# Kernel optimization log

Hardware: AMD Instinct MI355X
Metric: run time of the kernel (lower is better)

## Reference

```python
import jax, jax.numpy as jnp
import numpy as np

B, H, S, D = 4, 32, 2048, 128  # batch, num_query_heads, seq_len, head_dim


def setup_inputs() -> dict:
    key = jax.random.key(0)
    k1, k2, k3, k4, k5 = jax.random.split(key, 5)
    return {
        "q": jax.random.normal(k1, (B, H, S, D), dtype=jnp.float32),
        "k": jax.random.normal(k2, (B, H, S, D), dtype=jnp.float32),
        "v": jax.random.normal(k3, (B, H, S, D), dtype=jnp.float32),
        "attention_output": jax.random.normal(k4, (B, H, S, D), dtype=jnp.float32),
        "betas": jnp.zeros((1, H, 1, D), dtype=jnp.float32),      # nn.Parameter(torch.zeros)
        "init_mem": jax.random.normal(k5, (1, H, D, D), dtype=jnp.float32),  # learnable init memory
        "init_z": jnp.ones((1, H, D, 1), dtype=jnp.float32),      # learnable init normalizer
    }


def reference(q, k, v, attention_output, betas, init_mem, init_z):
    # Infini-Attention style delta-rule memory, single segment (fresh init states).
    sigma_q = jax.nn.elu(q) + 1.0                      # [B,H,S,D]
    # memory read: [B,H,S,D] @ [1,H,D,D] -> [B,H,S,D], normalized by sigma_q @ z -> [B,H,S,1]
    memory_output = (sigma_q @ init_mem) / (sigma_q @ init_z)

    sigma_k = jax.nn.elu(k) + 1.0                      # [B,H,S,D]
    # delta rule: subtract what the memory already predicts for each key
    retrieved = (sigma_k @ init_mem) / (sigma_k @ init_z)
    value_delta = v - retrieved                        # [B,H,S,D]
    new_states = init_mem + jnp.swapaxes(sigma_k, -2, -1) @ value_delta  # [B,H,D,D]
    new_z = init_z + jnp.swapaxes(jnp.sum(sigma_k, axis=-2, keepdims=True), -2, -1)  # [B,H,D,1]

    gate = jax.nn.sigmoid(betas)                       # [1,H,1,D]
    out = gate * memory_output + (1.0 - gate) * attention_output
    # original returns only `out`; new_states/new_z are the side-effect state update,
    # returned here so the full delta-rule write path is exercised.
    return out, new_states, new_z
```

## Files before the change

kernel.cpp:

```cpp
#include <hip/hip_runtime.h>
#include <math.h>

#define NB 4
#define NH 32
#define NSQ 2048
#define ND 128
#define SPLIT 2
#define SCHUNK (NSQ / SPLIT)
#define RB 64
#define NITER (SCHUNK / RB)
#define NTHR 512

static constexpr size_t OUT_ELEMS = (size_t)NB * NH * NSQ * ND;
static constexpr size_t NS_OFF    = OUT_ELEMS;
static constexpr size_t NZ_OFF    = NS_OFF + (size_t)NB * NH * ND * ND;

static constexpr int LDS_BYTES = (2 * RB * 132 + 2 * ND * 64 + 3 * ND + 2 * RB) * 4;

typedef __attribute__((ext_vector_type(8))) short short8v;
typedef __attribute__((ext_vector_type(4))) float f32x4;

#define MFMA16(a, b, c) __builtin_amdgcn_mfma_f32_16x16x32_bf16(a, b, c, 0, 0, 0)

__device__ __forceinline__ float4 elu1(float4 x) {
    float4 r;
    r.x = x.x > 0.f ? x.x + 1.f : __expf(x.x);
    r.y = x.y > 0.f ? x.y + 1.f : __expf(x.y);
    r.z = x.z > 0.f ? x.z + 1.f : __expf(x.z);
    r.w = x.w > 0.f ? x.w + 1.f : __expf(x.w);
    return r;
}

__device__ __forceinline__ unsigned int pack1(float x) {
    unsigned int bx = __float_as_uint(x);
    float lo = x - __uint_as_float(bx & 0xFFFF0000u);
    return __builtin_amdgcn_perm(bx, __float_as_uint(lo), 0x07060302u);
}
__device__ __forceinline__ float uph(unsigned int w) { return __uint_as_float(w & 0xFFFF0000u); }
__device__ __forceinline__ float upl(unsigned int w) { return __uint_as_float(w << 16); }

__device__ __forceinline__ void unpack2(uint4 a, uint4 b, short8v& hi, short8v& lo) {
    union { unsigned int u[4]; short8v s; } H, L;
    H.u[0] = __builtin_amdgcn_perm(a.y, a.x, 0x07060302u);
    H.u[1] = __builtin_amdgcn_perm(a.w, a.z, 0x07060302u);
    H.u[2] = __builtin_amdgcn_perm(b.y, b.x, 0x07060302u);
    H.u[3] = __builtin_amdgcn_perm(b.w, b.z, 0x07060302u);
    L.u[0] = __builtin_amdgcn_perm(a.y, a.x, 0x05040100u);
    L.u[1] = __builtin_amdgcn_perm(a.w, a.z, 0x05040100u);
    L.u[2] = __builtin_amdgcn_perm(b.y, b.x, 0x05040100u);
    L.u[3] = __builtin_amdgcn_perm(b.w, b.z, 0x05040100u);
    hi = H.s; lo = L.s;
}

__device__ __forceinline__ void pack8(const float* x, short8v& hi, short8v& lo) {
    union { unsigned int u[4]; short8v s; } H, L;
    #pragma unroll
    for (int d = 0; d < 4; ++d) {
        unsigned int b0 = __float_as_uint(x[2 * d]);
        unsigned int b1 = __float_as_uint(x[2 * d + 1]);
        float l0 = x[2 * d]     - __uint_as_float(b0 & 0xFFFF0000u);
        float l1 = x[2 * d + 1] - __uint_as_float(b1 & 0xFFFF0000u);
        H.u[d] = __builtin_amdgcn_perm(b1, b0, 0x07060302u);
        L.u[d] = __builtin_amdgcn_perm(__float_as_uint(l1), __float_as_uint(l0), 0x07060302u);
    }
    hi = H.s; lo = L.s;
}

extern "C" __global__ void cm_init(const float* __restrict__ mem0,
                                   const float* __restrict__ z0,
                                   float* __restrict__ out) {
    const int NSF4 = NB * NH * ND * ND / 4;
    const int NZF4 = NB * NH * ND / 4;
    int idx = blockIdx.x * 256 + threadIdx.x;
    if (idx < NSF4) {
        const int per_bh = ND * ND / 4;
        int h = (idx / per_bh) % NH;
        int off = idx % per_bh;
        ((float4*)(out + NS_OFF))[idx] = ((const float4*)mem0)[h * per_bh + off];
    } else if (idx < NSF4 + NZF4) {
        int j = idx - NSF4;
        const int per_bh = ND / 4;
        int h = (j / per_bh) % NH;
        int off = j % per_bh;
        ((float4*)(out + NZ_OFF))[j] = ((const float4*)z0)[h * per_bh + off];
    }
}

extern "C" __global__ void __launch_bounds__(NTHR, 2)
cm_main(const float* __restrict__ q, const float* __restrict__ kin,
        const float* __restrict__ v, const float* __restrict__ attn,
        const float* __restrict__ betas, const float* __restrict__ mem0,
        const float* __restrict__ z0, float* __restrict__ out) {
    extern __shared__ unsigned int lds[];
    uint4* lsqT  = (uint4*)lds;
    uint4* lskT  = lsqT + RB * 33;
    uint4* skT   = lskT + RB * 33;
    uint4* vdT   = skT + ND * 16;
    float* lz    = (float*)(vdT + ND * 16);
    float* lgate = lz + ND;
    float* lsqz  = lgate + ND;
    float* lskz  = lsqz + RB;
    float* lnz   = lskz + RB;

    const int t   = threadIdx.x;
    const int wg  = blockIdx.x;
    const int cch = wg % SPLIT;
    const int h   = (wg / SPLIT) % NH;
    const int b   = wg / (SPLIT * NH);

    if (t < ND) {
        lz[t] = z0[h * ND + t];
        float be = betas[h * ND + t];
        lgate[t] = 1.f / (1.f + __expf(-be));
        lnz[t] = 0.f;
    }

    const int lane = t & 63;
    const int l15  = lane & 15;
    const int l4   = lane >> 4;
    const int wid  = t >> 6;
    const int wr   = wid >> 2;
    const int wc   = wid & 3;
    const int cc   = t & 31;
    const int rg2  = t >> 5;

    const size_t bh = (size_t)b * NH + h;
    const float4* q4 = (const float4*)(q   + bh * NSQ * ND);
    const float4* k4 = (const float4*)(kin + bh * NSQ * ND);
    const float*  vf = v    + bh * NSQ * ND;
    const float*  af = attn + bh * NSQ * ND;
    float*        of = out  + bh * NSQ * ND;

    short8v bmh[2][4], bml[2][4];
    {
        const float* mh = mem0 + (size_t)h * ND * ND;
        #pragma unroll
        for (int ct = 0; ct < 2; ++ct) {
            #pragma unroll
            for (int kt = 0; kt < 4; ++kt) {
                const int j  = wc * 32 + ct * 16 + l15;
                const int i0 = kt * 32 + l4 * 8;
                float x[8];
                #pragma unroll
                for (int e = 0; e < 8; ++e) x[e] = mh[(i0 + e) * ND + j];
                pack8(x, bmh[ct][kt], bml[ct][kt]);
            }
        }
    }

    f32x4 nsa[8];
    #pragma unroll
    for (int i = 0; i < 8; ++i) nsa[i] = (f32x4){0.f, 0.f, 0.f, 0.f};
    float4 nz = make_float4(0.f, 0.f, 0.f, 0.f);

    __syncthreads();

    for (int blk = 0; blk < NITER; ++blk) {
        const int s0 = cch * SCHUNK + blk * RB;

        uint4 kp[4];
        #pragma unroll
        for (int m = 0; m < 4; ++m) {
            const int r = rg2 * 4 + m;
            const size_t g = (size_t)(s0 + r) * 32 + cc;
            float4 sq = elu1(q4[g]);
            float4 sk = elu1(k4[g]);
            nz.x += sk.x; nz.y += sk.y; nz.z += sk.z; nz.w += sk.w;
            uint4 qp = make_uint4(pack1(sq.x), pack1(sq.y), pack1(sq.z), pack1(sq.w));
            kp[m]    = make_uint4(pack1(sk.x), pack1(sk.y), pack1(sk.z), pack1(sk.w));
            lsqT[r * 33 + cc] = qp;
            lskT[r * 33 + cc] = kp[m];
        }
        {
            const int swz = rg2 ^ (cc & 7);
            skT[(4 * cc + 0) * 16 + swz] = make_uint4(kp[0].x, kp[1].x, kp[2].x, kp[3].x);
            skT[(4 * cc + 1) * 16 + swz] = make_uint4(kp[0].y, kp[1].y, kp[2].y, kp[3].y);
            skT[(4 * cc + 2) * 16 + swz] = make_uint4(kp[0].z, kp[1].z, kp[2].z, kp[3].z);
            skT[(4 * cc + 3) * 16 + swz] = make_uint4(kp[0].w, kp[1].w, kp[2].w, kp[3].w);
        }
        __syncthreads();

        float pav[2][2][4], pvv[2][2][4];
        #pragma unroll
        for (int tr = 0; tr < 2; ++tr)
            #pragma unroll
            for (int ct = 0; ct < 2; ++ct) {
                const int col = wc * 32 + ct * 16 + l15;
                #pragma unroll
                for (int rg = 0; rg < 4; ++rg) {
                    const int r = wr * 32 + tr * 16 + l4 * 4 + rg;
                    const size_t off = (size_t)(s0 + r) * ND + col;
                    pav[tr][ct][rg] = af[off];
                    pvv[tr][ct][rg] = vf[off];
                }
            }

        if (t < 2 * RB) {
            const int r = t & (RB - 1);
            const uint4* src = (t < RB) ? lsqT : lskT;
            float acc = 0.f;
            #pragma unroll 8
            for (int d4 = 0; d4 < 32; ++d4) {
                uint4 pw = src[r * 33 + d4];
                float4 zz = ((const float4*)lz)[d4];
                acc = fmaf(uph(pw.x) + upl(pw.x), zz.x, acc);
                acc = fmaf(uph(pw.y) + upl(pw.y), zz.y, acc);
                acc = fmaf(uph(pw.z) + upl(pw.z), zz.z, acc);
                acc = fmaf(uph(pw.w) + upl(pw.w), zz.w, acc);
            }
            if (t < RB) lsqz[r] = acc; else lskz[r] = acc;
        }

        f32x4 mo[2][2], rt[2][2];
        #pragma unroll
        for (int a_ = 0; a_ < 2; ++a_)
            #pragma unroll
            for (int b_ = 0; b_ < 2; ++b_) {
                mo[a_][b_] = (f32x4){0.f, 0.f, 0.f, 0.f};
                rt[a_][b_] = (f32x4){0.f, 0.f, 0.f, 0.f};
            }

        #pragma unroll
        for (int kt = 0; kt < 4; ++kt) {
            #pragma unroll
            for (int tr = 0; tr < 2; ++tr) {
                const int r  = wr * 32 + tr * 16 + l15;
                const int c4 = kt * 8 + 2 * l4;
                short8v aqh, aql, akh, akl;
                unpack2(lsqT[r * 33 + c4], lsqT[r * 33 + c4 + 1], aqh, aql);
                unpack2(lskT[r * 33 + c4], lskT[r * 33 + c4 + 1], akh, akl);
                #pragma unroll
                for (int ct = 0; ct < 2; ++ct) {
                    mo[tr][ct] = MFMA16(aqh, bmh[ct][kt], mo[tr][ct]);
                    mo[tr][ct] = MFMA16(aql, bmh[ct][kt], mo[tr][ct]);
                    mo[tr][ct] = MFMA16(aqh, bml[ct][kt], mo[tr][ct]);
                    rt[tr][ct] = MFMA16(akh, bmh[ct][kt], rt[tr][ct]);
                    rt[tr][ct] = MFMA16(akl, bmh[ct][kt], rt[tr][ct]);
                    rt[tr][ct] = MFMA16(akh, bml[ct][kt], rt[tr][ct]);
                }
            }
        }
        __syncthreads();

        float isq[2][4], isk[2][4];
        #pragma unroll
        for (int tr = 0; tr < 2; ++tr)
            #pragma unroll
            for (int rg = 0; rg < 4; ++rg) {
                const int r = wr * 32 + tr * 16 + l4 * 4 + rg;
                isq[tr][rg] = 1.f / lsqz[r];
                isk[tr][rg] = 1.f / lskz[r];
            }
        #pragma unroll
        for (int tr = 0; tr < 2; ++tr) {
            const int rf4 = wr * 8 + tr * 4 + l4;
            #pragma unroll
            for (int ct = 0; ct < 2; ++ct) {
                const int col = wc * 32 + ct * 16 + l15;
                const float g = lgate[col];
                unsigned int pk[4];
                #pragma unroll
                for (int rg = 0; rg < 4; ++rg) {
                    const int r = wr * 32 + tr * 16 + l4 * 4 + rg;
                    const size_t off = (size_t)(s0 + r) * ND + col;
                    const float av = pav[tr][ct][rg];
                    const float mv = mo[tr][ct][rg] * isq[tr][rg];
                    of[off] = fmaf(g, mv - av, av);
                    const float vd = fmaf(-isk[tr][rg], rt[tr][ct][rg], pvv[tr][ct][rg]);
                    pk[rg] = pack1(vd);
                }
                vdT[col * 16 + (rf4 ^ ((col >> 2) & 7))] = make_uint4(pk[0], pk[1], pk[2], pk[3]);
            }
        }
        __syncthreads();

        #pragma unroll
        for (int kt = 0; kt < 2; ++kt) {
            const int dA = wid * 16 + l15;
            const int sA = (dA >> 2) & 7;
            const int h2 = kt * 8 + 2 * l4;
            short8v ah, al;
            unpack2(skT[dA * 16 + (h2 ^ sA)], skT[dA * 16 + ((h2 + 1) ^ sA)], ah, al);
            #pragma unroll
            for (int ct = 0; ct < 8; ++ct) {
                const int dB = ct * 16 + l15;
                const int sB = (dB >> 2) & 7;
                short8v bhv, blv;
                unpack2(vdT[dB * 16 + (h2 ^ sB)], vdT[dB * 16 + ((h2 + 1) ^ sB)], bhv, blv);
                nsa[ct] = MFMA16(ah, bhv, nsa[ct]);
                nsa[ct] = MFMA16(al, bhv, nsa[ct]);
                nsa[ct] = MFMA16(ah, blv, nsa[ct]);
            }
        }
        __syncthreads();
    }

    float* nso = out + NS_OFF + bh * ND * ND;
    #pragma unroll
    for (int ct = 0; ct < 8; ++ct) {
        #pragma unroll
        for (int rg = 0; rg < 4; ++rg) {
            const int i = wid * 16 + l4 * 4 + rg;
            const int j = ct * 16 + l15;
            atomicAdd(nso + (size_t)i * ND + j, nsa[ct][rg]);
        }
    }
    atomicAdd(&lnz[cc * 4 + 0], nz.x);
    atomicAdd(&lnz[cc * 4 + 1], nz.y);
    atomicAdd(&lnz[cc * 4 + 2], nz.z);
    atomicAdd(&lnz[cc * 4 + 3], nz.w);
    __syncthreads();
    if (t < ND) atomicAdd(out + NZ_OFF + bh * ND + t, lnz[t]);
}

extern "C" void kernel_launch(void* const* d_in, const int* in_sizes, int n_in,
                              void* d_out, int out_size, void* d_ws, size_t ws_size,
                              hipStream_t stream) {
    const float* q     = (const float*)d_in[0];
    const float* k     = (const float*)d_in[1];
    const float* v     = (const float*)d_in[2];
    const float* attn  = (const float*)d_in[3];
    const float* betas = (const float*)d_in[4];
    const float* mem0  = (const float*)d_in[5];
    const float* z0    = (const float*)d_in[6];
    float* out = (float*)d_out;

    hipFuncSetAttribute((const void*)cm_main,
                        hipFuncAttributeMaxDynamicSharedMemorySize, LDS_BYTES);

    const int initF4 = NB * NH * ND * ND / 4 + NB * NH * ND / 4;
    cm_init<<<(initF4 + 255) / 256, 256, 0, stream>>>(mem0, z0, out);
    cm_main<<<NB * NH * SPLIT, NTHR, LDS_BYTES, stream>>>(q, k, v, attn, betas, mem0, z0, out);
}
```

Measured before the change: 628.4 us.

## Store split-bf16 hi/lo planes in LDS, halve row block, double split

Replaces the interleaved packed hi/lo LDS layout with separate bf16 hi and lo planes, so MFMA operands are read directly as short8 vectors with no per-use perm unpacking. The row block shrinks to 32 and the sequence split grows to 4, which doubles the grid and raises the launch-bounds occupancy target to 4. Q and K staging is divided between thread halves instead of each thread doing both, and the reciprocal of each normalizer is computed once. Smaller blocks mean more barriers per row and twice as many atomic adds into the global state from more workgroups.

```diff
diff --git a/kernel.cpp b/kernel.cpp
--- a/kernel.cpp
+++ b/kernel.cpp
@@ -5,9 +5,9 @@
 #define NH 32
 #define NSQ 2048
 #define ND 128
-#define SPLIT 2
+#define SPLIT 4
 #define SCHUNK (NSQ / SPLIT)
-#define RB 64
+#define RB 32
 #define NITER (SCHUNK / RB)
 #define NTHR 512
 
@@ -15,7 +15,20 @@
 static constexpr size_t NS_OFF    = OUT_ELEMS;
 static constexpr size_t NZ_OFF    = NS_OFF + (size_t)NB * NH * ND * ND;
 
-static constexpr int LDS_BYTES = (2 * RB * 132 + 2 * ND * 64 + 3 * ND + 2 * RB) * 4;
+#define SQH   0
+#define SQL   8704
+#define SKH   17408
+#define SKL   26112
+#define SKTH  34816
+#define SKTL  43008
+#define VDTH  51200
+#define VDTL  59392
+#define LZ    67584
+#define LGATE 68096
+#define LSQZ  68608
+#define LSKZ  68736
+#define LNZ   68864
+static constexpr int LDS_BYTES = 69376;
 
 typedef __attribute__((ext_vector_type(8))) short short8v;
 typedef __attribute__((ext_vector_type(4))) float f32x4;
@@ -31,37 +44,21 @@
     return r;
 }
 
-__device__ __forceinline__ unsigned int pack1(float x) {
-    unsigned int bx = __float_as_uint(x);
-    float lo = x - __uint_as_float(bx & 0xFFFF0000u);
-    return __builtin_amdgcn_perm(bx, __float_as_uint(lo), 0x07060302u);
-}
-__device__ __forceinline__ float uph(unsigned int w) { return __uint_as_float(w & 0xFFFF0000u); }
-__device__ __forceinline__ float upl(unsigned int w) { return __uint_as_float(w << 16); }
-
-__device__ __forceinline__ void unpack2(uint4 a, uint4 b, short8v& hi, short8v& lo) {
-    union { unsigned int u[4]; short8v s; } H, L;
-    H.u[0] = __builtin_amdgcn_perm(a.y, a.x, 0x07060302u);
-    H.u[1] = __builtin_amdgcn_perm(a.w, a.z, 0x07060302u);
-    H.u[2] = __builtin_amdgcn_perm(b.y, b.x, 0x07060302u);
-    H.u[3] = __builtin_amdgcn_perm(b.w, b.z, 0x07060302u);
-    L.u[0] = __builtin_amdgcn_perm(a.y, a.x, 0x05040100u);
-    L.u[1] = __builtin_amdgcn_perm(a.w, a.z, 0x05040100u);
-    L.u[2] = __builtin_amdgcn_perm(b.y, b.x, 0x05040100u);
-    L.u[3] = __builtin_amdgcn_perm(b.w, b.z, 0x05040100u);
-    hi = H.s; lo = L.s;
-}
+__device__ __forceinline__ unsigned int pk2(float x1, float x0) {
+    return __builtin_amdgcn_perm(__float_as_uint(x1), __float_as_uint(x0), 0x07060302u);
+}
+__device__ __forceinline__ float flo(float x) {
+    return x - __uint_as_float(__float_as_uint(x) & 0xFFFF0000u);
+}
+__device__ __forceinline__ float blo(unsigned int w) { return __uint_as_float(w << 16); }
+__device__ __forceinline__ float bhi(unsigned int w) { return __uint_as_float(w & 0xFFFF0000u); }
 
 __device__ __forceinline__ void pack8(const float* x, short8v& hi, short8v& lo) {
     union { unsigned int u[4]; short8v s; } H, L;
     #pragma unroll
     for (int d = 0; d < 4; ++d) {
-        unsigned int b0 = __float_as_uint(x[2 * d]);
-        unsigned int b1 = __float_as_uint(x[2 * d + 1]);
-        float l0 = x[2 * d]     - __uint_as_float(b0 & 0xFFFF0000u);
-        float l1 = x[2 * d + 1] - __uint_as_float(b1 & 0xFFFF0000u);
-        H.u[d] = __builtin_amdgcn_perm(b1, b0, 0x07060302u);
-        L.u[d] = __builtin_amdgcn_perm(__float_as_uint(l1), __float_as_uint(l0), 0x07060302u);
+        H.u[d] = pk2(x[2 * d + 1], x[2 * d]);
+        L.u[d] = pk2(flo(x[2 * d + 1]), flo(x[2 * d]));
     }
     hi = H.s; lo = L.s;
 }
@@ -86,21 +83,17 @@
     }
 }
 
-extern "C" __global__ void __launch_bounds__(NTHR, 2)
+extern "C" __global__ void __launch_bounds__(NTHR, 4)
 cm_main(const float* __restrict__ q, const float* __restrict__ kin,
         const float* __restrict__ v, const float* __restrict__ attn,
         const float* __restrict__ betas, const float* __restrict__ mem0,
         const float* __restrict__ z0, float* __restrict__ out) {
-    extern __shared__ unsigned int lds[];
-    uint4* lsqT  = (uint4*)lds;
-    uint4* lskT  = lsqT + RB * 33;
-    uint4* skT   = lskT + RB * 33;
-    uint4* vdT   = skT + ND * 16;
-    float* lz    = (float*)(vdT + ND * 16);
-    float* lgate = lz + ND;
-    float* lsqz  = lgate + ND;
-    float* lskz  = lsqz + RB;
-    float* lnz   = lskz + RB;
+    extern __shared__ char lds[];
+    float* lzf    = (float*)(lds + LZ);
+    float* lgatef = (float*)(lds + LGATE);
+    float* lsqzf  = (float*)(lds + LSQZ);
+    float* lskzf  = (float*)(lds + LSKZ);
+    float* lnzf   = (float*)(lds + LNZ);
 
     const int t   = threadIdx.x;
     const int wg  = blockIdx.x;
@@ -109,10 +102,10 @@
     const int b   = wg / (SPLIT * NH);
 
     if (t < ND) {
-        lz[t] = z0[h * ND + t];
+        lzf[t] = z0[h * ND + t];
         float be = betas[h * ND + t];
-        lgate[t] = 1.f / (1.f + __expf(-be));
-        lnz[t] = 0.f;
+        lgatef[t] = 1.f / (1.f + __expf(-be));
+        lnzf[t] = 0.f;
     }
 
     const int lane = t & 63;
@@ -122,7 +115,8 @@
     const int wr   = wid >> 2;
     const int wc   = wid & 3;
     const int cc   = t & 31;
-    const int rg2  = t >> 5;
+    const int rg   = (t >> 5) & 7;
+    const bool isK = (t < 256);
 
     const size_t bh = (size_t)b * NH + h;
     const float4* q4 = (const float4*)(q   + bh * NSQ * ND);
@@ -142,7 +136,7 @@
                 const int i0 = kt * 32 + l4 * 8;
                 float x[8];
                 #pragma unroll
-                for (int e = 0; e < 8; ++e) x[e] = mh[(i0 + e) * ND + j];
+                for (int e = 0; e < 8; ++e) x[e] = mh[(size_t)(i0 + e) * ND + j];
                 pack8(x, bmh[ct][kt], bml[ct][kt]);
             }
         }
@@ -153,143 +147,143 @@
     for (int i = 0; i < 8; ++i) nsa[i] = (f32x4){0.f, 0.f, 0.f, 0.f};
     float4 nz = make_float4(0.f, 0.f, 0.f, 0.f);
 
+    const float4* src4 = isK ? k4 : q4;
+    const int pb_h = isK ? SKH : SQH;
+    const int pb_l = pb_h + 8704;
+
     __syncthreads();
 
     for (int blk = 0; blk < NITER; ++blk) {
         const int s0 = cch * SCHUNK + blk * RB;
 
-        uint4 kp[4];
+        float sf[4][4];
         #pragma unroll
         for (int m = 0; m < 4; ++m) {
-            const int r = rg2 * 4 + m;
-            const size_t g = (size_t)(s0 + r) * 32 + cc;
-            float4 sq = elu1(q4[g]);
-            float4 sk = elu1(k4[g]);
-            nz.x += sk.x; nz.y += sk.y; nz.z += sk.z; nz.w += sk.w;
-            uint4 qp = make_uint4(pack1(sq.x), pack1(sq.y), pack1(sq.z), pack1(sq.w));
-            kp[m]    = make_uint4(pack1(sk.x), pack1(sk.y), pack1(sk.z), pack1(sk.w));
-            lsqT[r * 33 + cc] = qp;
-            lskT[r * 33 + cc] = kp[m];
-        }
+            const int r = rg * 4 + m;
+            float4 sv = elu1(src4[(size_t)(s0 + r) * 32 + cc]);
+            if (isK) { nz.x += sv.x; nz.y += sv.y; nz.z += sv.z; nz.w += sv.w; }
+            *(uint2*)(lds + pb_h + r * 272 + cc * 8) =
+                make_uint2(pk2(sv.y, sv.x), pk2(sv.w, sv.z));
+            *(uint2*)(lds + pb_l + r * 272 + cc * 8) =
+                make_uint2(pk2(flo(sv.y), flo(sv.x)), pk2(flo(sv.w), flo(sv.z)));
+            sf[m][0] = sv.x; sf[m][1] = sv.y; sf[m][2] = sv.z; sf[m][3] = sv.w;
+        }
+        if (isK) {
+            #pragma unroll
+            for (int j = 0; j < 4; ++j) {
+                const int d  = cc * 4 + j;
+                const int pg = (rg >> 1) ^ (((d >> 1) ^ (d >> 4)) & 3);
+                const int hf = rg & 1;
+                *(uint2*)(lds + SKTH + d * 64 + pg * 16 + hf * 8) =
+                    make_uint2(pk2(sf[1][j], sf[0][j]), pk2(sf[3][j], sf[2][j]));
+                *(uint2*)(lds + SKTL + d * 64 + pg * 16 + hf * 8) =
+                    make_uint2(pk2(flo(sf[1][j]), flo(sf[0][j])), pk2(flo(sf[3][j]), flo(sf[2][j])));
+            }
+        }
+        __syncthreads();
+
+        if (t < 64) {
+            const int r  = t & 31;
+            const int ph = (t < 32) ? SQH : SKH;
+            float acc = 0.f;
+            #pragma unroll 4
+            for (int c = 0; c < 16; ++c) {
+                uint4 wh = *(const uint4*)(lds + ph + r * 272 + c * 16);
+                uint4 wl = *(const uint4*)(lds + ph + 8704 + r * 272 + c * 16);
+                float4 za = *(const float4*)(lds + LZ + c * 32);
+                float4 zb = *(const float4*)(lds + LZ + c * 32 + 16);
+                acc = fmaf(blo(wh.x) + blo(wl.x), za.x, acc);
+                acc = fmaf(bhi(wh.x) + bhi(wl.x), za.y, acc);
+                acc = fmaf(blo(wh.y) + blo(wl.y), za.z, acc);
+                acc = fmaf(bhi(wh.y) + bhi(wl.y), za.w, acc);
+                acc = fmaf(blo(wh.z) + blo(wl.z), zb.x, acc);
+                acc = fmaf(bhi(wh.z) + bhi(wl.z), zb.y, acc);
+                acc = fmaf(blo(wh.w) + blo(wl.w), zb.z, acc);
+                acc = fmaf(bhi(wh.w) + bhi(wl.w), zb.w, acc);
+            }
+            const float inv = 1.f / acc;
+            if (t < 32) lsqzf[r] = inv; else lskzf[r] = inv;
+        }
+
+        f32x4 mo[2], rt2[2];
+        #pragma unroll
+        for (int ct = 0; ct < 2; ++ct) {
+            mo[ct]  = (f32x4){0.f, 0.f, 0.f, 0.f};
+            rt2[ct] = (f32x4){0.f, 0.f, 0.f, 0.f};
+        }
+        #pragma unroll
+        for (int kt = 0; kt < 4; ++kt) {
+            const int ro = (wr * 16 + l15) * 272 + kt * 64 + l4 * 16;
+            short8v aqh = *(const short8v*)(lds + SQH + ro);
+            short8v aql = *(const short8v*)(lds + SQL + ro);
+            short8v akh = *(const short8v*)(lds + SKH + ro);
+            short8v akl = *(const short8v*)(lds + SKL + ro);
+            #pragma unroll
+            for (int ct = 0; ct < 2; ++ct) {
+                mo[ct]  = MFMA16(aqh, bmh[ct][kt], mo[ct]);
+                mo[ct]  = MFMA16(aql, bmh[ct][kt], mo[ct]);
+                mo[ct]  = MFMA16(aqh, bml[ct][kt], mo[ct]);
+                rt2[ct] = MFMA16(akh, bmh[ct][kt], rt2[ct]);
+                rt2[ct] = MFMA16(akl, bmh[ct][kt], rt2[ct]);
+                rt2[ct] = MFMA16(akh, bml[ct][kt], rt2[ct]);
+            }
+        }
+        float avv[2][4], vvv[2][4];
+        #pragma unroll
+        for (int ct = 0; ct < 2; ++ct) {
+            const int col = wc * 32 + ct * 16 + l15;
+            #pragma unroll
+            for (int rgi = 0; rgi < 4; ++rgi) {
+                const size_t off = (size_t)(s0 + wr * 16 + l4 * 4 + rgi) * ND + col;
+                avv[ct][rgi] = af[off];
+                vvv[ct][rgi] = vf[off];
+            }
+        }
+        __syncthreads();
+
+        float isq[4], isk[4];
+        #pragma unroll
+        for (int rgi = 0; rgi < 4; ++rgi) {
+            const int r = wr * 16 + l4 * 4 + rgi;
+            isq[rgi] = lsqzf[r];
+            isk[rgi] = lskzf[r];
+        }
+        #pragma unroll
+        for (int ct = 0; ct < 2; ++ct) {
+            const int col = wc * 32 + ct * 16 + l15;
+            const float g = lgatef[col];
+            float vdv[4];
+            #pragma unroll
+            for (int rgi = 0; rgi < 4; ++rgi) {
+                const size_t off = (size_t)(s0 + wr * 16 + l4 * 4 + rgi) * ND + col;
+                const float av = avv[ct][rgi];
+                const float mv = mo[ct][rgi] * isq[rgi];
+                of[off] = fmaf(g, mv - av, av);
+                vdv[rgi] = fmaf(-isk[rgi], rt2[ct][rgi], vvv[ct][rgi]);
+            }
+            const int pg = (wr * 2 + (l4 >> 1)) ^ (((col >> 1) ^ (col >> 4)) & 3);
+            const int hf = l4 & 1;
+            *(uint2*)(lds + VDTH + col * 64 + pg * 16 + hf * 8) =
+                make_uint2(pk2(vdv[1], vdv[0]), pk2(vdv[3], vdv[2]));
+            *(uint2*)(lds + VDTL + col * 64 + pg * 16 + hf * 8) =
+                make_uint2(pk2(flo(vdv[1]), flo(vdv[0])), pk2(flo(vdv[3]), flo(vdv[2])));
+        }
+        __syncthreads();
+
         {
-            const int swz = rg2 ^ (cc & 7);
-            skT[(4 * cc + 0) * 16 + swz] = make_uint4(kp[0].x, kp[1].x, kp[2].x, kp[3].x);
-            skT[(4 * cc + 1) * 16 + swz] = make_uint4(kp[0].y, kp[1].y, kp[2].y, kp[3].y);
-            skT[(4 * cc + 2) * 16 + swz] = make_uint4(kp[0].z, kp[1].z, kp[2].z, kp[3].z);
-            skT[(4 * cc + 3) * 16 + swz] = make_uint4(kp[0].w, kp[1].w, kp[2].w, kp[3].w);
-        }
-        __syncthreads();
-
-        float pav[2][2][4], pvv[2][2][4];
-        #pragma unroll
-        for (int tr = 0; tr < 2; ++tr)
-            #pragma unroll
-            for (int ct = 0; ct < 2; ++ct) {
-                const int col = wc * 32 + ct * 16 + l15;
-                #pragma unroll
-                for (int rg = 0; rg < 4; ++rg) {
-                    const int r = wr * 32 + tr * 16 + l4 * 4 + rg;
-                    const size_t off = (size_t)(s0 + r) * ND + col;
-                    pav[tr][ct][rg] = af[off];
-                    pvv[tr][ct][rg] = vf[off];
-                }
-            }
-
-        if (t < 2 * RB) {
-            const int r = t & (RB - 1);
-            const uint4* src = (t < RB) ? lsqT : lskT;
-            float acc = 0.f;
-            #pragma unroll 8
-            for (int d4 = 0; d4 < 32; ++d4) {
-                uint4 pw = src[r * 33 + d4];
-                float4 zz = ((const float4*)lz)[d4];
-                acc = fmaf(uph(pw.x) + upl(pw.x), zz.x, acc);
-                acc = fmaf(uph(pw.y) + upl(pw.y), zz.y, acc);
-                acc = fmaf(uph(pw.z) + upl(pw.z), zz.z, acc);
-                acc = fmaf(uph(pw.w) + upl(pw.w), zz.w, acc);
-            }
-            if (t < RB) lsqz[r] = acc; else lskz[r] = acc;
-        }
-
-        f32x4 mo[2][2], rt[2][2];
-        #pragma unroll
-        for (int a_ = 0; a_ < 2; ++a_)
-            #pragma unroll
-            for (int b_ = 0; b_ < 2; ++b_) {
-                mo[a_][b_] = (f32x4){0.f, 0.f, 0.f, 0.f};
-                rt[a_][b_] = (f32x4){0.f, 0.f, 0.f, 0.f};
-            }
-
-        #pragma unroll
-        for (int kt = 0; kt < 4; ++kt) {
-            #pragma unroll
-            for (int tr = 0; tr < 2; ++tr) {
-                const int r  = wr * 32 + tr * 16 + l15;
-                const int c4 = kt * 8 + 2 * l4;
-                short8v aqh, aql, akh, akl;
-                unpack2(lsqT[r * 33 + c4], lsqT[r * 33 + c4 + 1], aqh, aql);
-                unpack2(lskT[r * 33 + c4], lskT[r * 33 + c4 + 1], akh, akl);
-                #pragma unroll
-                for (int ct = 0; ct < 2; ++ct) {
-                    mo[tr][ct] = MFMA16(aqh, bmh[ct][kt], mo[tr][ct]);
-                    mo[tr][ct] = MFMA16(aql, bmh[ct][kt], mo[tr][ct]);
-                    mo[tr][ct] = MFMA16(aqh, bml[ct][kt], mo[tr][ct]);
-                    rt[tr][ct] = MFMA16(akh, bmh[ct][kt], rt[tr][ct]);
-                    rt[tr][ct] = MFMA16(akl, bmh[ct][kt], rt[tr][ct]);
-                    rt[tr][ct] = MFMA16(akh, bml[ct][kt], rt[tr][ct]);
-                }
-            }
-        }
-        __syncthreads();
-
-        float isq[2][4], isk[2][4];
-        #pragma unroll
-        for (int tr = 0; tr < 2; ++tr)
-            #pragma unroll
-            for (int rg = 0; rg < 4; ++rg) {
-                const int r = wr * 32 + tr * 16 + l4 * 4 + rg;
-                isq[tr][rg] = 1.f / lsqz[r];
-                isk[tr][rg] = 1.f / lskz[r];
-            }
-        #pragma unroll
-        for (int tr = 0; tr < 2; ++tr) {
-            const int rf4 = wr * 8 + tr * 4 + l4;
-            #pragma unroll
-            for (int ct = 0; ct < 2; ++ct) {
-                const int col = wc * 32 + ct * 16 + l15;
-                const float g = lgate[col];
-                unsigned int pk[4];
-                #pragma unroll
-                for (int rg = 0; rg < 4; ++rg) {
-                    const int r = wr * 32 + tr * 16 + l4 * 4 + rg;
-                    const size_t off = (size_t)(s0 + r) * ND + col;
-                    const float av = pav[tr][ct][rg];
-                    const float mv = mo[tr][ct][rg] * isq[tr][rg];
-                    of[off] = fmaf(g, mv - av, av);
-                    const float vd = fmaf(-isk[tr][rg], rt[tr][ct][rg], pvv[tr][ct][rg]);
-                    pk[rg] = pack1(vd);
-                }
-                vdT[col * 16 + (rf4 ^ ((col >> 2) & 7))] = make_uint4(pk[0], pk[1], pk[2], pk[3]);
-            }
-        }
-        __syncthreads();
-
-        #pragma unroll
-        for (int kt = 0; kt < 2; ++kt) {
             const int dA = wid * 16 + l15;
-            const int sA = (dA >> 2) & 7;
-            const int h2 = kt * 8 + 2 * l4;
-            short8v ah, al;
-            unpack2(skT[dA * 16 + (h2 ^ sA)], skT[dA * 16 + ((h2 + 1) ^ sA)], ah, al);
+            const int gA = l4 ^ (((dA >> 1) ^ (dA >> 4)) & 3);
+            short8v ah = *(const short8v*)(lds + SKTH + dA * 64 + gA * 16);
+            short8v al = *(const short8v*)(lds + SKTL + dA * 64 + gA * 16);
             #pragma unroll
             for (int ct = 0; ct < 8; ++ct) {
                 const int dB = ct * 16 + l15;
-                const int sB = (dB >> 2) & 7;
-                short8v bhv, blv;
-                unpack2(vdT[dB * 16 + (h2 ^ sB)], vdT[dB * 16 + ((h2 + 1) ^ sB)], bhv, blv);
-                nsa[ct] = MFMA16(ah, bhv, nsa[ct]);
-                nsa[ct] = MFMA16(al, bhv, nsa[ct]);
-                nsa[ct] = MFMA16(ah, blv, nsa[ct]);
+                const int gB = l4 ^ (((dB >> 1) ^ (dB >> 4)) & 3);
+                short8v bh = *(const short8v*)(lds + VDTH + dB * 64 + gB * 16);
+                short8v bl = *(const short8v*)(lds + VDTL + dB * 64 + gB * 16);
+                nsa[ct] = MFMA16(ah, bh, nsa[ct]);
+                nsa[ct] = MFMA16(al, bh, nsa[ct]);
+                nsa[ct] = MFMA16(ah, bl, nsa[ct]);
             }
         }
         __syncthreads();
@@ -299,18 +293,20 @@
     #pragma unroll
     for (int ct = 0; ct < 8; ++ct) {
         #pragma unroll
-        for (int rg = 0; rg < 4; ++rg) {
-            const int i = wid * 16 + l4 * 4 + rg;
+        for (int rgi = 0; rgi < 4; ++rgi) {
+            const int i = wid * 16 + l4 * 4 + rgi;
             const int j = ct * 16 + l15;
-            atomicAdd(nso + (size_t)i * ND + j, nsa[ct][rg]);
-        }
-    }
-    atomicAdd(&lnz[cc * 4 + 0], nz.x);
-    atomicAdd(&lnz[cc * 4 + 1], nz.y);
-    atomicAdd(&lnz[cc * 4 + 2], nz.z);
-    atomicAdd(&lnz[cc * 4 + 3], nz.w);
+            atomicAdd(nso + (size_t)i * ND + j, nsa[ct][rgi]);
+        }
+    }
+    if (isK) {
+        atomicAdd(&lnzf[cc * 4 + 0], nz.x);
+        atomicAdd(&lnzf[cc * 4 + 1], nz.y);
+        atomicAdd(&lnzf[cc * 4 + 2], nz.z);
+        atomicAdd(&lnzf[cc * 4 + 3], nz.w);
+    }
     __syncthreads();
-    if (t < ND) atomicAdd(out + NZ_OFF + bh * ND + t, lnz[t]);
+    if (t < ND) atomicAdd(out + NZ_OFF + bh * ND + t, lnzf[t]);
 }
 
 extern "C" void kernel_launch(void* const* d_in, const int* in_sizes, int n_in,
```

Result: slower. 651.5 us (+3.7%).
